# Optimization experiments

Hardware: AMD Instinct MI355X
Metric: run time of the kernel (lower is better)

The kernel has to match this reference:

```python
import jax, jax.numpy as jnp
import numpy as np

NUM_Q_HEADS = 32
NUM_KV_HEADS = 8
HEAD_DIM = 128
HIDDEN = 4096
EPS = 1e-6
ROPE_THETA = 1e6


def _rmsnorm(t, w):
    # per-head RMSNorm over last dim (head_dim), as in skip_rmsnorm with residual=None
    var = jnp.mean(t * t, axis=-1, keepdims=True)
    return t * jax.lax.rsqrt(var + EPS) * w


def _rotate_half(t):
    h = t.shape[-1] // 2
    return jnp.concatenate([-t[..., h:], t[..., :h]], axis=-1)


def setup_inputs() -> dict:
    key = jax.random.key(0)
    ks = jax.random.split(key, 4)
    B, S = 2, 1024
    x = jax.random.normal(ks[0], (B, S, HIDDEN), jnp.float32)
    q_proj_w = jax.random.normal(ks[1], (HIDDEN, NUM_Q_HEADS * HEAD_DIM), jnp.float32) * 0.02
    kv_proj_w = jax.random.normal(ks[2], (HIDDEN, 2 * NUM_KV_HEADS * HEAD_DIM), jnp.float32) * 0.02
    o_proj_w = jax.random.normal(ks[3], (NUM_Q_HEADS * HEAD_DIM, HIDDEN), jnp.float32) * 0.02
    q_norm_w = jnp.ones((HEAD_DIM,), jnp.float32)
    k_norm_w = jnp.ones((HEAD_DIM,), jnp.float32)
    # real rotate-half RoPE tables, shape [S, head_dim]
    inv_freq = 1.0 / (ROPE_THETA ** (jnp.arange(0, HEAD_DIM, 2, dtype=jnp.float32) / HEAD_DIM))
    freqs = jnp.arange(S, dtype=jnp.float32)[:, None] * inv_freq[None, :]  # [S, hd/2]
    emb = jnp.concatenate([freqs, freqs], axis=-1)  # [S, hd]
    cos, sin = jnp.cos(emb), jnp.sin(emb)
    kv_buffer = jnp.zeros((16384, 2 * NUM_KV_HEADS, HEAD_DIM), jnp.float32)
    cur_select_index = jnp.arange(B * S, dtype=jnp.int32)
    return {"x": x, "q_proj_w": q_proj_w, "kv_proj_w": kv_proj_w, "o_proj_w": o_proj_w,
            "q_norm_w": q_norm_w, "k_norm_w": k_norm_w, "cos": cos, "sin": sin,
            "kv_buffer": kv_buffer, "cur_select_index": cur_select_index}


def reference(x, q_proj_w, kv_proj_w, o_proj_w, q_norm_w, k_norm_w, cos, sin, kv_buffer, cur_select_index):
    B, S, _ = x.shape
    T = B * S
    xf = x.reshape(T, HIDDEN)
    # projections (weights stored as [in, out])
    xq = (xf @ q_proj_w).reshape(T, NUM_Q_HEADS, HEAD_DIM)
    xkv = xf @ kv_proj_w
    xk = xkv[:, : NUM_KV_HEADS * HEAD_DIM].reshape(T, NUM_KV_HEADS, HEAD_DIM)
    xv = xkv[:, NUM_KV_HEADS * HEAD_DIM:].reshape(T, NUM_KV_HEADS, HEAD_DIM)
    # per-head RMSNorm (Qwen3 q/k norm)
    xq = _rmsnorm(xq, q_norm_w)
    xk = _rmsnorm(xk, k_norm_w)
    # RoPE (cos/sin are [S, hd], tiled over batch, broadcast over heads)
    cos_t = jnp.tile(cos, (B, 1))[:, None, :]  # [T,1,hd]
    sin_t = jnp.tile(sin, (B, 1))[:, None, :]
    xq = xq * cos_t + _rotate_half(xq) * sin_t
    xk = xk * cos_t + _rotate_half(xk) * sin_t
    # paged KV-cache scatter update (update_kv_buffer)
    combined_kv = jnp.concatenate([xk, xv], axis=1)  # [T, 2*Hk, hd]
    buf = kv_buffer.at[cur_select_index].set(combined_kv)
    # ragged causal flash attention (equal per-request lengths here), GQA expand
    rep = NUM_Q_HEADS // NUM_KV_HEADS
    q = xq.reshape(B, S, NUM_Q_HEADS, HEAD_DIM)
    k = jnp.repeat(xk.reshape(B, S, NUM_KV_HEADS, HEAD_DIM), rep, axis=2)
    v = jnp.repeat(xv.reshape(B, S, NUM_KV_HEADS, HEAD_DIM), rep, axis=2)
    scale = HEAD_DIM ** -0.5
    scores = jnp.einsum('bqhd,bkhd->bhqk', q, k) * scale  # [B,H,S,S]
    causal = jnp.tril(jnp.ones((S, S), bool))
    scores = jnp.where(causal[None, None], scores, jnp.float32(-1e30))
    p = jax.nn.softmax(scores, axis=-1)
    attn = jnp.einsum('bhqk,bkhd->bqhd', p, v).reshape(B, S, NUM_Q_HEADS * HEAD_DIM)
    out = attn @ o_proj_w  # [B,S,hidden]
    return out, buf
```

## Files before the change

### kernel.cpp

```cpp
#include <hip/hip_runtime.h>

typedef float fx4 __attribute__((ext_vector_type(4)));
typedef short s16x4 __attribute__((ext_vector_type(4)));
typedef short s16x8 __attribute__((ext_vector_type(8)));
typedef __bf16 bf16x8 __attribute__((ext_vector_type(8)));

__device__ __forceinline__ short f2bf(float f) {
  unsigned u = __builtin_bit_cast(unsigned, f);
  u += 0x7fffu + ((u >> 16) & 1u);
  return (short)(u >> 16);
}

__device__ __forceinline__ bf16x8 ld8(const short* p) {
  s16x8 v = *(const s16x8*)p;
  return __builtin_bit_cast(bf16x8, v);
}

__device__ __forceinline__ void gld16(const void* g, void* l) {
  __builtin_amdgcn_global_load_lds(
      (const __attribute__((address_space(1))) unsigned*)g,
      (__attribute__((address_space(3))) unsigned*)l, 16, 0, 0);
}

__global__ __launch_bounds__(256) void cvt_k(const float* __restrict__ in,
                                             short* __restrict__ out) {
  int i = (blockIdx.x * 256 + threadIdx.x) * 8;
  fx4 a = *(const fx4*)(in + i);
  fx4 b = *(const fx4*)(in + i + 4);
  s16x8 w;
  w[0] = f2bf(a[0]); w[1] = f2bf(a[1]); w[2] = f2bf(a[2]); w[3] = f2bf(a[3]);
  w[4] = f2bf(b[0]); w[5] = f2bf(b[1]); w[6] = f2bf(b[2]); w[7] = f2bf(b[3]);
  *(s16x8*)(out + i) = w;
}

__global__ __launch_bounds__(256) void tr_k(const float* __restrict__ in,
    short* __restrict__ out, int K, int N) {
  __shared__ short T[64][72];
  const int ktiles = K >> 6;
  const int tk0 = (blockIdx.x % ktiles) << 6;
  const int tn0 = (blockIdx.x / ktiles) << 6;
  const int tid = threadIdx.x;
  #pragma unroll
  for (int i = 0; i < 4; ++i) {
    int idx = i * 256 + tid;
    int k = idx >> 4, n4 = (idx & 15) << 2;
    fx4 v = *(const fx4*)(in + (size_t)(tk0 + k) * N + tn0 + n4);
    #pragma unroll
    for (int j = 0; j < 4; ++j) T[n4 + j][k] = f2bf(v[j]);
  }
  __syncthreads();
  #pragma unroll
  for (int i = 0; i < 2; ++i) {
    int idx = i * 256 + tid;
    int n = idx >> 3, k8 = (idx & 7) << 3;
    *(s16x8*)(out + (size_t)(tn0 + n) * K + tk0 + k8) = *(const s16x8*)&T[n][k8];
  }
}

__global__ __launch_bounds__(256) void vtr_k(const short* __restrict__ vbp,
                                             short* __restrict__ vbt) {
  __shared__ short T[64][72];
  const int tile = blockIdx.x & 31;
  const int tt = tile & 15, dt = tile >> 4;
  const int bk = blockIdx.x >> 5;
  const int b = bk >> 3, kvh = bk & 7;
  const int t0 = tt << 6, d0 = dt << 6;
  const int tid = threadIdx.x;
  #pragma unroll
  for (int i = 0; i < 2; ++i) {
    int idx = i * 256 + tid;
    int r = idx >> 3, c8 = (idx & 7) << 3;
    s16x8 v = *(const s16x8*)(vbp + (size_t)(b * 1024 + t0 + r) * 1024 + kvh * 128 + d0 + c8);
    #pragma unroll
    for (int j = 0; j < 8; ++j) T[c8 + j][r] = v[j];
  }
  __syncthreads();
  #pragma unroll
  for (int i = 0; i < 2; ++i) {
    int idx = i * 256 + tid;
    int r = idx >> 3, c8 = (idx & 7) << 3;
    *(s16x8*)(vbt + ((size_t)(b * 8 + kvh) * 128 + d0 + r) * 1024 + t0 + c8) =
        *(const s16x8*)&T[r][c8];
  }
}

__global__ __launch_bounds__(256) void gemm_k(const short* __restrict__ A,
    const short* __restrict__ Bt, float* __restrict__ Cp, int N, int K) {
  __shared__ short As[2][128 * 64];
  __shared__ short Bs[2][128 * 64];
  const int tiles_n = N >> 7;
  const int tm = blockIdx.x / tiles_n, tn = blockIdx.x % tiles_n;
  const int tid = threadIdx.x;
  const int lane = tid & 63, wv = tid >> 6;
  const int wr = (wv >> 1) << 6, wc = (wv & 1) << 6;
  const int r0 = tm << 7, c0 = tn << 7;
  const int lrow = lane & 15, lg = lane >> 4;
  const int srow = tid >> 3, sch = tid & 7;
  fx4 acc[4][4] = {};

  auto stage = [&](int buf, int k0) {
    #pragma unroll
    for (int i = 0; i < 4; ++i) {
      int row = (i << 5) + srow;
      int gk = ((sch ^ (row & 7)) << 3);
      gld16(A + (size_t)(r0 + row) * K + k0 + gk, &As[buf][(i * 256 + wv * 64) * 8]);
    }
    #pragma unroll
    for (int i = 0; i < 4; ++i) {
      int row = (i << 5) + srow;
      int gk = ((sch ^ (row & 7)) << 3);
      gld16(Bt + (size_t)(c0 + row) * K + k0 + gk, &Bs[buf][(i * 256 + wv * 64) * 8]);
    }
  };

  const int nt = K >> 6;
  stage(0, 0);
  __syncthreads();
  int cur = 0;
  for (int t = 0; t < nt; ++t) {
    if (t + 1 < nt) stage(cur ^ 1, (t + 1) << 6);
    bf16x8 af[4][2], bfr[4][2];
    #pragma unroll
    for (int m = 0; m < 4; ++m) {
      int row = wr + m * 16 + lrow;
      #pragma unroll
      for (int h = 0; h < 2; ++h)
        af[m][h] = ld8(&As[cur][row * 64 + ((((h << 2) + lg) ^ (row & 7)) << 3)]);
    }
    #pragma unroll
    for (int n = 0; n < 4; ++n) {
      int row = wc + n * 16 + lrow;
      #pragma unroll
      for (int h = 0; h < 2; ++h)
        bfr[n][h] = ld8(&Bs[cur][row * 64 + ((((h << 2) + lg) ^ (row & 7)) << 3)]);
    }
    __builtin_amdgcn_s_setprio(1);
    #pragma unroll
    for (int m = 0; m < 4; ++m)
      #pragma unroll
      for (int n = 0; n < 4; ++n) {
        acc[m][n] = __builtin_amdgcn_mfma_f32_16x16x32_bf16(af[m][0], bfr[n][0], acc[m][n], 0, 0, 0);
        acc[m][n] = __builtin_amdgcn_mfma_f32_16x16x32_bf16(af[m][1], bfr[n][1], acc[m][n], 0, 0, 0);
      }
    __builtin_amdgcn_s_setprio(0);
    __syncthreads();
    cur ^= 1;
  }
  const int g4 = lg << 2;
  #pragma unroll
  for (int m = 0; m < 4; ++m)
    #pragma unroll
    for (int n = 0; n < 4; ++n)
      #pragma unroll
      for (int j = 0; j < 4; ++j) {
        int row = r0 + wr + m * 16 + g4 + j;
        int col = c0 + wc + n * 16 + lrow;
        Cp[(size_t)row * N + col] = acc[m][n][j];
      }
}

__global__ __launch_bounds__(256) void nr_k(const float* __restrict__ xqkv,
    const float* __restrict__ qnw, const float* __restrict__ knw,
    const float* __restrict__ cosb, const float* __restrict__ sinb,
    const int* __restrict__ idx,
    short* __restrict__ qb, short* __restrict__ kbp, short* __restrict__ vbp,
    float* __restrict__ bufo) {
  int rid = blockIdx.x * 4 + (threadIdx.x >> 6);
  int l = threadIdx.x & 63;
  int type, t, h;
  if (rid < 65536)      { type = 0; t = rid >> 5; h = rid & 31; }
  else if (rid < 81920) { type = 1; int r = rid - 65536; t = r >> 3; h = r & 7; }
  else                  { type = 2; int r = rid - 81920; t = r >> 3; h = r & 7; }
  int s = t & 1023;
  const float* src = xqkv + (size_t)t * 6144 +
                     ((type == 0) ? h * 128 : (type == 1) ? 4096 + h * 128
                                                          : 5120 + h * 128);
  float e0 = src[l], e1 = src[l + 64];
  float out0, out1;
  if (type < 2) {
    float ss = e0 * e0 + e1 * e1;
    #pragma unroll
    for (int off = 1; off < 64; off <<= 1) ss += __shfl_xor(ss, off);
    float r = rsqrtf(ss * (1.0f / 128.0f) + 1e-6f);
    const float* nw = (type == 0) ? qnw : knw;
    float n0 = e0 * r * nw[l], n1 = e1 * r * nw[l + 64];
    float c0 = cosb[s * 128 + l], c1 = cosb[s * 128 + 64 + l];
    float s0 = sinb[s * 128 + l], s1 = sinb[s * 128 + 64 + l];
    out0 = n0 * c0 - n1 * s0;
    out1 = n1 * c1 + n0 * s1;
  } else { out0 = e0; out1 = e1; }
  if (type == 0) {
    short* d = qb + (size_t)t * 4096 + h * 128;
    d[l] = f2bf(out0); d[l + 64] = f2bf(out1);
  } else {
    int br = idx[t];
    float* bd = bufo + (size_t)br * 2048 + (type == 1 ? 0 : 1024) + h * 128;
    bd[l] = out0; bd[l + 64] = out1;
    short* d = (type == 1) ? kbp + (size_t)t * 1024 + h * 128
                           : vbp + (size_t)t * 1024 + h * 128;
    d[l] = f2bf(out0); d[l + 64] = f2bf(out1);
  }
}

#define KLD 136
#define PLD 72

__global__ __launch_bounds__(256) void attn_k(const short* __restrict__ qb,
    const short* __restrict__ kbp, const short* __restrict__ vbt,
    short* __restrict__ ob) {
  __shared__ short Ks[64 * KLD];
  __shared__ short Vs[128 * 64];
  __shared__ short Ps[4][16 * PLD];
  const int bid = blockIdx.x;
  const int qt = 15 - (bid & 15), h = (bid >> 4) & 31, b = bid >> 9;
  const int kvh = h >> 2;
  const int tid = threadIdx.x, lane = tid & 63, w = tid >> 6;
  const int lrow = lane & 15, lg = lane >> 4, lk = lg << 3;
  const int q0 = qt << 6;
  const float SC2 = 0.088388347648318447f * 1.4426950408889634f;

  bf16x8 qf[4];
  {
    const short* qp = qb + ((size_t)(b * 1024 + q0 + w * 16 + lrow) * 32 + h) * 128 + lk;
    #pragma unroll
    for (int kb4 = 0; kb4 < 4; ++kb4) qf[kb4] = ld8(qp + kb4 * 32);
  }

  const short* vt_base = vbt + (size_t)(b * 8 + kvh) * 128 * 1024;

  const int sr = tid >> 4, sd8 = (tid & 15) << 3;
  const int vdr = tid >> 3, vch = tid & 7;
  s16x8 kreg[4], vreg[4];
  auto ldkv = [&](int kv0) {
    #pragma unroll
    for (int it = 0; it < 4; ++it) {
      int r = (it << 4) + sr;
      kreg[it] = *(const s16x8*)(kbp + ((size_t)(b * 1024 + kv0 + r) * 8 + kvh) * 128 + sd8);
      int d = (it << 5) + vdr;
      vreg[it] = *(const s16x8*)(vt_base + (size_t)d * 1024 + kv0 + (vch << 3));
    }
  };
  auto wrkv = [&]() {
    #pragma unroll
    for (int it = 0; it < 4; ++it) {
      int r = (it << 4) + sr;
      *(s16x8*)&Ks[r * KLD + sd8] = kreg[it];
      int d = (it << 5) + vdr;
      *(s16x8*)&Vs[d * 64 + ((vch ^ (d & 7)) << 3)] = vreg[it];
    }
  };

  float m[4], lsum[4];
  fx4 acc[8] = {};
  #pragma unroll
  for (int j = 0; j < 4; ++j) { m[j] = -3.0e38f; lsum[j] = 0.f; }

  ldkv(0);
  wrkv();
  __syncthreads();

  for (int kt = 0; kt <= qt; ++kt) {
    const int kv0 = kt << 6;
    if (kt < qt) ldkv((kt + 1) << 6);
    fx4 sf[4];
    #pragma unroll
    for (int nc = 0; nc < 4; ++nc) {
      fx4 z = {0.f, 0.f, 0.f, 0.f};
      sf[nc] = z;
      #pragma unroll
      for (int kb4 = 0; kb4 < 4; ++kb4) {
        bf16x8 kf = ld8(&Ks[(nc * 16 + lrow) * KLD + kb4 * 32 + lk]);
        sf[nc] = __builtin_amdgcn_mfma_f32_16x16x32_bf16(qf[kb4], kf, sf[nc], 0, 0, 0);
      }
    }
    if (kt == qt) {
      #pragma unroll
      for (int nc = 0; nc < 4; ++nc)
        #pragma unroll
        for (int j = 0; j < 4; ++j) {
          int qr = q0 + w * 16 + (lg << 2) + j;
          int kc = kv0 + nc * 16 + lrow;
          if (kc > qr) sf[nc][j] = -3.0e38f;
        }
    }
    float pm[4];
    #pragma unroll
    for (int j = 0; j < 4; ++j) pm[j] = -3.0e38f;
    #pragma unroll
    for (int nc = 0; nc < 4; ++nc)
      #pragma unroll
      for (int j = 0; j < 4; ++j) pm[j] = fmaxf(pm[j], sf[nc][j]);
    #pragma unroll
    for (int j = 0; j < 4; ++j) {
      pm[j] = fmaxf(pm[j], __shfl_xor(pm[j], 1));
      pm[j] = fmaxf(pm[j], __shfl_xor(pm[j], 2));
      pm[j] = fmaxf(pm[j], __shfl_xor(pm[j], 4));
      pm[j] = fmaxf(pm[j], __shfl_xor(pm[j], 8));
    }
    float alpha[4], rs[4];
    #pragma unroll
    for (int j = 0; j < 4; ++j) {
      float mn = fmaxf(m[j], pm[j]);
      alpha[j] = exp2f((m[j] - mn) * SC2);
      m[j] = mn;
      rs[j] = 0.f;
    }
    #pragma unroll
    for (int nc = 0; nc < 4; ++nc)
      #pragma unroll
      for (int j = 0; j < 4; ++j) {
        float p = exp2f((sf[nc][j] - m[j]) * SC2);
        rs[j] += p;
        Ps[w][((lg << 2) + j) * PLD + nc * 16 + lrow] = f2bf(p);
      }
    #pragma unroll
    for (int j = 0; j < 4; ++j) {
      rs[j] += __shfl_xor(rs[j], 1);
      rs[j] += __shfl_xor(rs[j], 2);
      rs[j] += __shfl_xor(rs[j], 4);
      rs[j] += __shfl_xor(rs[j], 8);
      lsum[j] = lsum[j] * alpha[j] + rs[j];
    }
    #pragma unroll
    for (int dg = 0; dg < 8; ++dg)
      #pragma unroll
      for (int j = 0; j < 4; ++j) acc[dg][j] *= alpha[j];
    #pragma unroll
    for (int kb2 = 0; kb2 < 2; ++kb2) {
      bf16x8 pf = ld8(&Ps[w][lrow * PLD + kb2 * 32 + lk]);
      #pragma unroll
      for (int dg = 0; dg < 8; ++dg) {
        int d = dg * 16 + lrow;
        int tch = (kb2 << 2) + lg;
        bf16x8 vf = ld8(&Vs[d * 64 + ((tch ^ (d & 7)) << 3)]);
        acc[dg] = __builtin_amdgcn_mfma_f32_16x16x32_bf16(pf, vf, acc[dg], 0, 0, 0);
      }
    }
    __syncthreads();
    if (kt < qt) {
      wrkv();
      __syncthreads();
    }
  }
  #pragma unroll
  for (int j = 0; j < 4; ++j) {
    float rl = 1.0f / lsum[j];
    int t = b * 1024 + q0 + w * 16 + (lg << 2) + j;
    short* op = ob + ((size_t)t * 32 + h) * 128;
    #pragma unroll
    for (int dg = 0; dg < 8; ++dg)
      op[dg * 16 + lrow] = f2bf(acc[dg][j] * rl);
  }
}

extern "C" void kernel_launch(void* const* d_in, const int* in_sizes, int n_in,
                              void* d_out, int out_size, void* d_ws, size_t ws_size,
                              hipStream_t stream) {
  (void)in_sizes; (void)n_in; (void)out_size; (void)ws_size;
  const float* x    = (const float*)d_in[0];
  const float* qw   = (const float*)d_in[1];
  const float* kvw  = (const float*)d_in[2];
  const float* ow   = (const float*)d_in[3];
  const float* qnw  = (const float*)d_in[4];
  const float* knw  = (const float*)d_in[5];
  const float* cosb = (const float*)d_in[6];
  const float* sinb = (const float*)d_in[7];
  const float* kvbf = (const float*)d_in[8];
  const int*   idx  = (const int*)d_in[9];

  float* outp = (float*)d_out;
  float* bufp = outp + (size_t)2048 * 4096;

  char* ws = (char*)d_ws;
  float* xqkv = (float*)ws;
  short* qb   = (short*)(ws + (size_t)2048 * 6144 * 4);
  short* kbp  = (short*)((char*)qb + (size_t)2048 * 4096 * 2);
  short* vbp  = (short*)((char*)kbp + (size_t)2048 * 1024 * 2);
  short* attnb = (short*)xqkv;
  short* owt   = (short*)((char*)xqkv + (size_t)2048 * 4096 * 2);
  short* vbt   = owt;

  short* wqkvt = (short*)bufp;
  short* xb    = (short*)((char*)bufp + (size_t)6144 * 4096 * 2);

  cvt_k<<<dim3(4096), dim3(256), 0, stream>>>(x, xb);
  tr_k<<<dim3(64 * 64), dim3(256), 0, stream>>>(qw, wqkvt, 4096, 4096);
  tr_k<<<dim3(64 * 32), dim3(256), 0, stream>>>(kvw, wqkvt + (size_t)4096 * 4096, 4096, 2048);
  gemm_k<<<dim3(16 * 48), dim3(256), 0, stream>>>(xb, wqkvt, xqkv, 6144, 4096);
  hipMemcpyAsync(bufp + (size_t)2048 * 2048, kvbf + (size_t)2048 * 2048,
                 (size_t)(16384 - 2048) * 2048 * 4, hipMemcpyDeviceToDevice, stream);
  nr_k<<<dim3(98304 / 4), dim3(256), 0, stream>>>(xqkv, qnw, knw, cosb, sinb, idx,
                                                  qb, kbp, vbp, bufp);
  vtr_k<<<dim3(512), dim3(256), 0, stream>>>(vbp, vbt);
  attn_k<<<dim3(2 * 32 * 16), dim3(256), 0, stream>>>(qb, kbp, vbt, attnb);
  tr_k<<<dim3(64 * 64), dim3(256), 0, stream>>>(ow, owt, 4096, 4096);
  gemm_k<<<dim3(16 * 32), dim3(256), 0, stream>>>(attnb, owt, outp, 4096, 4096);
}
```

Measured before the change: 429.2 us.

## Use triple-buffered 512-thread GEMM with explicit vmcnt waits and wider tiles

Replaces the double-buffered 256-thread GEMM with a templated 512-thread kernel that keeps three K-stages of async global-to-LDS loads in flight, using explicit vmcnt waits and raw barriers instead of __syncthreads. The QKV projection uses 128x192 tiles so its grid becomes 512 blocks, matching the output projection. The aim is to hide global load latency better and balance the grid across CUs. In exchange, LDS use is much higher and occupancy per CU is lower.

```diff
diff --git a/kernel.cpp b/kernel.cpp
--- a/kernel.cpp
+++ b/kernel.cpp
@@ -20,6 +20,15 @@
   __builtin_amdgcn_global_load_lds(
       (const __attribute__((address_space(1))) unsigned*)g,
       (__attribute__((address_space(3))) unsigned*)l, 16, 0, 0);
+}
+
+template<int N> __device__ __forceinline__ void wait_vmcnt() {
+  if constexpr (N == 0)       asm volatile("s_waitcnt vmcnt(0)" ::: "memory");
+  else if constexpr (N == 4)  asm volatile("s_waitcnt vmcnt(4)" ::: "memory");
+  else if constexpr (N == 5)  asm volatile("s_waitcnt vmcnt(5)" ::: "memory");
+  else if constexpr (N == 8)  asm volatile("s_waitcnt vmcnt(8)" ::: "memory");
+  else if constexpr (N == 10) asm volatile("s_waitcnt vmcnt(10)" ::: "memory");
+  __builtin_amdgcn_sched_barrier(0);
 }
 
 __global__ __launch_bounds__(256) void cvt_k(const float* __restrict__ in,
@@ -84,42 +93,55 @@
   }
 }
 
-__global__ __launch_bounds__(256) void gemm_k(const short* __restrict__ A,
+template<int BN>
+__global__ __launch_bounds__(512) void gemm_p(const short* __restrict__ A,
     const short* __restrict__ Bt, float* __restrict__ Cp, int N, int K) {
-  __shared__ short As[2][128 * 64];
-  __shared__ short Bs[2][128 * 64];
-  const int tiles_n = N >> 7;
+  constexpr int GB = BN / 64;
+  constexpr int G  = 2 + GB;
+  constexpr int NF = BN / 64;
+  constexpr int NWC = BN / 4;
+  __shared__ short As[3][128 * 64];
+  __shared__ short Bs[3][BN * 64];
+  const int tiles_n = N / BN;
   const int tm = blockIdx.x / tiles_n, tn = blockIdx.x % tiles_n;
   const int tid = threadIdx.x;
   const int lane = tid & 63, wv = tid >> 6;
-  const int wr = (wv >> 1) << 6, wc = (wv & 1) << 6;
-  const int r0 = tm << 7, c0 = tn << 7;
+  const int wr = (wv >> 2) << 6, wc = (wv & 3) * NWC;
+  const int r0 = tm << 7, c0 = tn * BN;
   const int lrow = lane & 15, lg = lane >> 4;
-  const int srow = tid >> 3, sch = tid & 7;
-  fx4 acc[4][4] = {};
+  fx4 acc[4][NF] = {};
 
   auto stage = [&](int buf, int k0) {
     #pragma unroll
-    for (int i = 0; i < 4; ++i) {
-      int row = (i << 5) + srow;
-      int gk = ((sch ^ (row & 7)) << 3);
-      gld16(A + (size_t)(r0 + row) * K + k0 + gk, &As[buf][(i * 256 + wv * 64) * 8]);
-    }
-    #pragma unroll
-    for (int i = 0; i < 4; ++i) {
-      int row = (i << 5) + srow;
-      int gk = ((sch ^ (row & 7)) << 3);
-      gld16(Bt + (size_t)(c0 + row) * K + k0 + gk, &Bs[buf][(i * 256 + wv * 64) * 8]);
+    for (int i = 0; i < 2; ++i) {
+      int c = i * 512 + tid;
+      int row = c >> 3, ch = c & 7;
+      gld16(A + (size_t)(r0 + row) * K + k0 + ((ch ^ (row & 7)) << 3),
+            &As[buf][(i * 512 + wv * 64) * 8]);
+    }
+    #pragma unroll
+    for (int i = 0; i < GB; ++i) {
+      int c = i * 512 + tid;
+      int row = c >> 3, ch = c & 7;
+      gld16(Bt + (size_t)(c0 + row) * K + k0 + ((ch ^ (row & 7)) << 3),
+            &Bs[buf][(i * 512 + wv * 64) * 8]);
     }
   };
 
   const int nt = K >> 6;
   stage(0, 0);
-  __syncthreads();
+  stage(1, 64);
+  stage(2, 128);
   int cur = 0;
   for (int t = 0; t < nt; ++t) {
-    if (t + 1 < nt) stage(cur ^ 1, (t + 1) << 6);
-    bf16x8 af[4][2], bfr[4][2];
+    int rem = nt - 1 - t;
+    if (rem >= 2)      wait_vmcnt<2 * G>();
+    else if (rem == 1) wait_vmcnt<G>();
+    else               wait_vmcnt<0>();
+    __builtin_amdgcn_s_barrier();
+    __builtin_amdgcn_sched_barrier(0);
+
+    bf16x8 af[4][2], bfr[NF][2];
     #pragma unroll
     for (int m = 0; m < 4; ++m) {
       int row = wr + m * 16 + lrow;
@@ -128,7 +150,7 @@
         af[m][h] = ld8(&As[cur][row * 64 + ((((h << 2) + lg) ^ (row & 7)) << 3)]);
     }
     #pragma unroll
-    for (int n = 0; n < 4; ++n) {
+    for (int n = 0; n < NF; ++n) {
       int row = wc + n * 16 + lrow;
       #pragma unroll
       for (int h = 0; h < 2; ++h)
@@ -138,19 +160,22 @@
     #pragma unroll
     for (int m = 0; m < 4; ++m)
       #pragma unroll
-      for (int n = 0; n < 4; ++n) {
+      for (int n = 0; n < NF; ++n) {
         acc[m][n] = __builtin_amdgcn_mfma_f32_16x16x32_bf16(af[m][0], bfr[n][0], acc[m][n], 0, 0, 0);
         acc[m][n] = __builtin_amdgcn_mfma_f32_16x16x32_bf16(af[m][1], bfr[n][1], acc[m][n], 0, 0, 0);
       }
     __builtin_amdgcn_s_setprio(0);
-    __syncthreads();
-    cur ^= 1;
+
+    __builtin_amdgcn_s_barrier();
+    __builtin_amdgcn_sched_barrier(0);
+    if (t + 3 < nt) stage(cur, (t + 3) << 6);
+    cur = (cur == 2) ? 0 : cur + 1;
   }
   const int g4 = lg << 2;
   #pragma unroll
   for (int m = 0; m < 4; ++m)
     #pragma unroll
-    for (int n = 0; n < 4; ++n)
+    for (int n = 0; n < NF; ++n)
       #pragma unroll
       for (int j = 0; j < 4; ++j) {
         int row = r0 + wr + m * 16 + g4 + j;
@@ -386,7 +411,7 @@
   cvt_k<<<dim3(4096), dim3(256), 0, stream>>>(x, xb);
   tr_k<<<dim3(64 * 64), dim3(256), 0, stream>>>(qw, wqkvt, 4096, 4096);
   tr_k<<<dim3(64 * 32), dim3(256), 0, stream>>>(kvw, wqkvt + (size_t)4096 * 4096, 4096, 2048);
-  gemm_k<<<dim3(16 * 48), dim3(256), 0, stream>>>(xb, wqkvt, xqkv, 6144, 4096);
+  gemm_p<192><<<dim3(512), dim3(512), 0, stream>>>(xb, wqkvt, xqkv, 6144, 4096);
   hipMemcpyAsync(bufp + (size_t)2048 * 2048, kvbf + (size_t)2048 * 2048,
                  (size_t)(16384 - 2048) * 2048 * 4, hipMemcpyDeviceToDevice, stream);
   nr_k<<<dim3(98304 / 4), dim3(256), 0, stream>>>(xqkv, qnw, knw, cosb, sinb, idx,
@@ -394,5 +419,5 @@
   vtr_k<<<dim3(512), dim3(256), 0, stream>>>(vbp, vbt);
   attn_k<<<dim3(2 * 32 * 16), dim3(256), 0, stream>>>(qb, kbp, vbt, attnb);
   tr_k<<<dim3(64 * 64), dim3(256), 0, stream>>>(ow, owt, 4096, 4096);
-  gemm_k<<<dim3(16 * 32), dim3(256), 0, stream>>>(attnb, owt, outp, 4096, 4096);
-}
+  gemm_p<128><<<dim3(512), dim3(512), 0, stream>>>(attnb, owt, outp, 4096, 4096);
+}
```

Result: slower. 476.0 us (+10.9%).

## Add 256x256 eight-wave GEMM with ping-pong staging for QKV projection

Applied to the files above, without the earlier changes.

Adds a 512-thread GEMM kernel with 256x256 output tiles split into four 128x128 quadrants. Global-to-LDS loads for later quadrants are interleaved with MFMA work on the current ones, using explicit vmcnt waits, barriers and setprio. The QKV projection now uses it, so there are fewer blocks (192) with more reuse per block. The risks are lower occupancy and the grid of 192 blocks not filling all compute units. The old gemm_k staging index math is also reworked without changing its semantics.

```diff
diff --git a/kernel.cpp b/kernel.cpp
--- a/kernel.cpp
+++ b/kernel.cpp
@@ -20,6 +20,17 @@
   __builtin_amdgcn_global_load_lds(
       (const __attribute__((address_space(1))) unsigned*)g,
       (__attribute__((address_space(3))) unsigned*)l, 16, 0, 0);
+}
+
+template<int N> __device__ __forceinline__ void wait_vmcnt() {
+  if constexpr (N == 0)      asm volatile("s_waitcnt vmcnt(0)" ::: "memory");
+  else if constexpr (N == 4) asm volatile("s_waitcnt vmcnt(4)" ::: "memory");
+  __builtin_amdgcn_sched_barrier(0);
+}
+
+__device__ __forceinline__ void barrier_pin() {
+  __builtin_amdgcn_s_barrier();
+  __builtin_amdgcn_sched_barrier(0);
 }
 
 __global__ __launch_bounds__(256) void cvt_k(const float* __restrict__ in,
@@ -82,6 +93,140 @@
     *(s16x8*)(vbt + ((size_t)(b * 8 + kvh) * 128 + d0 + r) * 1024 + t0 + c8) =
         *(const s16x8*)&T[r][c8];
   }
+}
+
+__global__ __launch_bounds__(512) void gemm8(const short* __restrict__ A,
+    const short* __restrict__ Bt, float* __restrict__ Cp, int N, int K) {
+  __shared__ short As[2][2][128 * 64];
+  __shared__ short Bs[2][2][128 * 64];
+  const int tiles_n = N >> 8;
+  const int tm = blockIdx.x / tiles_n, tn = blockIdx.x % tiles_n;
+  const int tid = threadIdx.x;
+  const int lane = tid & 63, wv = tid >> 6;
+  const int wm = (wv >> 2) << 6;
+  const int wn = (wv & 3) << 5;
+  const int r0 = tm << 8, c0 = tn << 8;
+  const int lrow = lane & 15, lg = lane >> 4;
+
+  auto stageA = [&](int t, int hh) {
+    int k0 = t << 6, s = t & 1;
+    #pragma unroll
+    for (int i = 0; i < 2; ++i) {
+      int c = i * 512 + tid;
+      int row = c >> 3, ch = c & 7;
+      gld16(A + (size_t)(r0 + hh * 128 + row) * K + k0 + ((ch ^ (row & 7)) << 3),
+            &As[s][hh][(i * 512 + wv * 64) * 8]);
+    }
+  };
+  auto stageB = [&](int t, int hh) {
+    int k0 = t << 6, s = t & 1;
+    #pragma unroll
+    for (int i = 0; i < 2; ++i) {
+      int c = i * 512 + tid;
+      int row = c >> 3, ch = c & 7;
+      gld16(Bt + (size_t)(c0 + hh * 128 + row) * K + k0 + ((ch ^ (row & 7)) << 3),
+            &Bs[s][hh][(i * 512 + wv * 64) * 8]);
+    }
+  };
+
+  fx4 acc[2][2][4][2] = {};
+  bf16x8 a[4][2], b[2][2];
+
+  auto ldA = [&](int s, int hh) {
+    #pragma unroll
+    for (int mf = 0; mf < 4; ++mf) {
+      int lr = wm + mf * 16 + lrow;
+      #pragma unroll
+      for (int ks = 0; ks < 2; ++ks)
+        a[mf][ks] = ld8(&As[s][hh][lr * 64 + ((((ks << 2) + lg) ^ (lr & 7)) << 3)]);
+    }
+  };
+  auto ldB = [&](int s, int hh) {
+    #pragma unroll
+    for (int nf = 0; nf < 2; ++nf) {
+      int lr = wn + nf * 16 + lrow;
+      #pragma unroll
+      for (int ks = 0; ks < 2; ++ks)
+        b[nf][ks] = ld8(&Bs[s][hh][lr * 64 + ((((ks << 2) + lg) ^ (lr & 7)) << 3)]);
+    }
+  };
+
+  const int nt = K >> 6;
+  stageA(0, 0); stageA(0, 1); stageB(0, 0); stageB(0, 1);
+  stageA(1, 0); stageB(1, 1);
+
+  for (int t = 0; t < nt; ++t) {
+    const int s = t & 1;
+    if (t + 1 < nt) wait_vmcnt<4>(); else wait_vmcnt<0>();
+    barrier_pin();
+    ldA(s, 0); ldB(s, 0);
+    if (t + 1 < nt) stageA(t + 1, 1);
+    __builtin_amdgcn_s_setprio(1);
+    #pragma unroll
+    for (int ks = 0; ks < 2; ++ks)
+      #pragma unroll
+      for (int mf = 0; mf < 4; ++mf)
+        #pragma unroll
+        for (int nf = 0; nf < 2; ++nf)
+          acc[0][0][mf][nf] = __builtin_amdgcn_mfma_f32_16x16x32_bf16(
+              a[mf][ks], b[nf][ks], acc[0][0][mf][nf], 0, 0, 0);
+    __builtin_amdgcn_s_setprio(0);
+    barrier_pin();
+    ldB(s, 1);
+    if (t + 1 < nt) stageB(t + 1, 0);
+    __builtin_amdgcn_s_setprio(1);
+    #pragma unroll
+    for (int ks = 0; ks < 2; ++ks)
+      #pragma unroll
+      for (int mf = 0; mf < 4; ++mf)
+        #pragma unroll
+        for (int nf = 0; nf < 2; ++nf)
+          acc[0][1][mf][nf] = __builtin_amdgcn_mfma_f32_16x16x32_bf16(
+              a[mf][ks], b[nf][ks], acc[0][1][mf][nf], 0, 0, 0);
+    __builtin_amdgcn_s_setprio(0);
+    barrier_pin();
+    ldA(s, 1);
+    if (t + 2 < nt) stageA(t + 2, 0);
+    __builtin_amdgcn_s_setprio(1);
+    #pragma unroll
+    for (int ks = 0; ks < 2; ++ks)
+      #pragma unroll
+      for (int mf = 0; mf < 4; ++mf)
+        #pragma unroll
+        for (int nf = 0; nf < 2; ++nf)
+          acc[1][1][mf][nf] = __builtin_amdgcn_mfma_f32_16x16x32_bf16(
+              a[mf][ks], b[nf][ks], acc[1][1][mf][nf], 0, 0, 0);
+    __builtin_amdgcn_s_setprio(0);
+    barrier_pin();
+    ldB(s, 0);
+    if (t + 2 < nt) stageB(t + 2, 1);
+    __builtin_amdgcn_s_setprio(1);
+    #pragma unroll
+    for (int ks = 0; ks < 2; ++ks)
+      #pragma unroll
+      for (int mf = 0; mf < 4; ++mf)
+        #pragma unroll
+        for (int nf = 0; nf < 2; ++nf)
+          acc[1][0][mf][nf] = __builtin_amdgcn_mfma_f32_16x16x32_bf16(
+              a[mf][ks], b[nf][ks], acc[1][0][mf][nf], 0, 0, 0);
+    __builtin_amdgcn_s_setprio(0);
+    barrier_pin();
+  }
+  const int g4 = lg << 2;
+  #pragma unroll
+  for (int mq = 0; mq < 2; ++mq)
+    #pragma unroll
+    for (int nq = 0; nq < 2; ++nq)
+      #pragma unroll
+      for (int mf = 0; mf < 4; ++mf)
+        #pragma unroll
+        for (int nf = 0; nf < 2; ++nf)
+          #pragma unroll
+          for (int j = 0; j < 4; ++j) {
+            int row = r0 + mq * 128 + wm + mf * 16 + g4 + j;
+            int col = c0 + nq * 128 + wn + nf * 16 + lrow;
+            Cp[(size_t)row * N + col] = acc[mq][nq][mf][nf][j];
+          }
 }
 
 __global__ __launch_bounds__(256) void gemm_k(const short* __restrict__ A,
@@ -95,21 +240,22 @@
   const int wr = (wv >> 1) << 6, wc = (wv & 1) << 6;
   const int r0 = tm << 7, c0 = tn << 7;
   const int lrow = lane & 15, lg = lane >> 4;
-  const int srow = tid >> 3, sch = tid & 7;
   fx4 acc[4][4] = {};
 
   auto stage = [&](int buf, int k0) {
     #pragma unroll
     for (int i = 0; i < 4; ++i) {
-      int row = (i << 5) + srow;
-      int gk = ((sch ^ (row & 7)) << 3);
-      gld16(A + (size_t)(r0 + row) * K + k0 + gk, &As[buf][(i * 256 + wv * 64) * 8]);
+      int c = i * 256 + tid;
+      int row = c >> 3, ch = c & 7;
+      gld16(A + (size_t)(r0 + row) * K + k0 + ((ch ^ (row & 7)) << 3),
+            &As[buf][(i * 256 + wv * 64) * 8]);
     }
     #pragma unroll
     for (int i = 0; i < 4; ++i) {
-      int row = (i << 5) + srow;
-      int gk = ((sch ^ (row & 7)) << 3);
-      gld16(Bt + (size_t)(c0 + row) * K + k0 + gk, &Bs[buf][(i * 256 + wv * 64) * 8]);
+      int c = i * 256 + tid;
+      int row = c >> 3, ch = c & 7;
+      gld16(Bt + (size_t)(c0 + row) * K + k0 + ((ch ^ (row & 7)) << 3),
+            &Bs[buf][(i * 256 + wv * 64) * 8]);
     }
   };
 
@@ -386,7 +532,7 @@
   cvt_k<<<dim3(4096), dim3(256), 0, stream>>>(x, xb);
   tr_k<<<dim3(64 * 64), dim3(256), 0, stream>>>(qw, wqkvt, 4096, 4096);
   tr_k<<<dim3(64 * 32), dim3(256), 0, stream>>>(kvw, wqkvt + (size_t)4096 * 4096, 4096, 2048);
-  gemm_k<<<dim3(16 * 48), dim3(256), 0, stream>>>(xb, wqkvt, xqkv, 6144, 4096);
+  gemm8<<<dim3(8 * 24), dim3(512), 0, stream>>>(xb, wqkvt, xqkv, 6144, 4096);
   hipMemcpyAsync(bufp + (size_t)2048 * 2048, kvbf + (size_t)2048 * 2048,
                  (size_t)(16384 - 2048) * 2048 * 4, hipMemcpyDeviceToDevice, stream);
   nr_k<<<dim3(98304 / 4), dim3(256), 0, stream>>>(xqkv, qnw, knw, cosb, sinb, idx,
```

After: 401.4 us. -6.5%, faster.
